# Kernel optimization log

Measured on AMD Instinct MI355X. Metric: run time of the kernel, lower is better.

The kernel has to match this reference:

```python
import jax, jax.numpy as jnp
import numpy as np

NUM_BINS = 31  # default num_bins in SummaryStats.from_array
N = 64 * 1024 * 1024  # 64M elements, 256 MB fp32 -> memory-bound reductions


def setup_inputs() -> dict:
    key = jax.random.key(0)
    x = jax.random.normal(key, (N,), dtype=jnp.float32)
    return {"x": x}


def reference(x):
    # SummaryStats.from_sharded_array on a single device (spec is fully replicated,
    # so _single_shard_histogram_array semantics apply: last bin is right-inclusive,
    # which matches jnp.histogram / searchsorted binning).
    x = x.ravel()
    mn = x.min()
    mx = x.max()
    nonzero_count = jnp.count_nonzero(x)
    num = jnp.asarray(x.size, dtype=nonzero_count.dtype)
    s = x.sum()
    ss = (x ** 2).sum()

    # histogram_bin_edges on stack([min, max]) with bins=NUM_BINS -> linspace(min, max, NUM_BINS+1)
    edges = jnp.linspace(mn, mx, NUM_BINS + 1)
    # bin index: values in [edges[i], edges[i+1]), last bin inclusive of edges[-1].
    idx = jnp.clip(jnp.searchsorted(edges, x, side="right") - 1, 0, NUM_BINS - 1)
    # exclude values strictly outside [min, max] (none here, but faithful to the compare logic)
    valid = (x >= edges[0]) & (x <= edges[-1])
    counts = jnp.zeros((NUM_BINS,), dtype=jnp.int32).at[idx].add(
        valid.astype(jnp.int32)
    )
    return mn, mx, num, nonzero_count, s, ss, counts, edges
```

## Files before the change

### kernel.cpp

```cpp
#include <hip/hip_runtime.h>

#define NBINS 31
#define NB1 2048
#define NB2 1024
#define PITCH 256

struct Partial {
    unsigned int mnk, mxk, nz, pad;
    double s, ss;
};
struct Finals {
    unsigned int minkey, maxkey;
    unsigned long long nz;
    double sum, ss;
};
#define OFF_F (NB1 * 32)
#define OFF_C (OFF_F + 64)

__device__ __forceinline__ unsigned int fkey(float f) {
    unsigned int u = __float_as_uint(f);
    return (u & 0x80000000u) ? ~u : (u | 0x80000000u);
}
__device__ __forceinline__ float funkey(unsigned int k) {
    return (k & 0x80000000u) ? __uint_as_float(k & 0x7FFFFFFFu)
                             : __uint_as_float(~k);
}
__device__ __forceinline__ float edge_at(float mn, float step, int i) {
    return __fadd_rn(mn, __fmul_rn((float)i, step));
}

__device__ __forceinline__ void acc4(float4 v, float& mn, float& mx, float& s, float& ss,
                                     unsigned int& nz) {
    mn = fminf(mn, fminf(fminf(v.x, v.y), fminf(v.z, v.w)));
    mx = fmaxf(mx, fmaxf(fmaxf(v.x, v.y), fmaxf(v.z, v.w)));
    s  += (v.x + v.y) + (v.z + v.w);
    ss += (v.x * v.x + v.y * v.y) + (v.z * v.z + v.w * v.w);
    nz += (v.x != 0.f) + (v.y != 0.f) + (v.z != 0.f) + (v.w != 0.f);
}

__global__ void __launch_bounds__(256) k_reduce(const float* __restrict__ x, long long n,
                                                Partial* __restrict__ part) {
    long long n4 = n >> 2;
    const float4* __restrict__ x4 = (const float4*)x;
    float mn = INFINITY, mx = -INFINITY, s = 0.f, ss = 0.f;
    unsigned int nz = 0u;

    long long stride = (long long)gridDim.x * blockDim.x;
    long long i = (long long)blockIdx.x * blockDim.x + threadIdx.x;
    for (; i + 3 * stride < n4; i += 4 * stride) {
        float4 a = x4[i], b = x4[i + stride], c = x4[i + 2 * stride], d = x4[i + 3 * stride];
        acc4(a, mn, mx, s, ss, nz);
        acc4(b, mn, mx, s, ss, nz);
        acc4(c, mn, mx, s, ss, nz);
        acc4(d, mn, mx, s, ss, nz);
    }
    for (; i < n4; i += stride) acc4(x4[i], mn, mx, s, ss, nz);
    if (blockIdx.x == 0 && threadIdx.x < (int)(n & 3)) {
        float v = x[(n4 << 2) + threadIdx.x];
        mn = fminf(mn, v); mx = fmaxf(mx, v);
        s += v; ss += v * v; nz += (v != 0.f);
    }

    double sd = (double)s, ssd = (double)ss;
    #pragma unroll
    for (int off = 32; off > 0; off >>= 1) {
        mn = fminf(mn, __shfl_down(mn, off));
        mx = fmaxf(mx, __shfl_down(mx, off));
        sd  += __shfl_down(sd, off);
        ssd += __shfl_down(ssd, off);
        nz  += __shfl_down(nz, off);
    }
    __shared__ float lmn[4], lmx[4];
    __shared__ double lsum[4], lss[4];
    __shared__ unsigned int lnz[4];
    int w = threadIdx.x >> 6;
    if ((threadIdx.x & 63) == 0) { lmn[w] = mn; lmx[w] = mx; lsum[w] = sd; lss[w] = ssd; lnz[w] = nz; }
    __syncthreads();
    if (threadIdx.x == 0) {
        Partial p;
        p.mnk = fkey(fminf(fminf(lmn[0], lmn[1]), fminf(lmn[2], lmn[3])));
        p.mxk = fkey(fmaxf(fmaxf(lmx[0], lmx[1]), fmaxf(lmx[2], lmx[3])));
        p.nz  = lnz[0] + lnz[1] + lnz[2] + lnz[3];
        p.pad = 0;
        p.s  = lsum[0] + lsum[1] + lsum[2] + lsum[3];
        p.ss = lss[0] + lss[1] + lss[2] + lss[3];
        part[blockIdx.x] = p;
    }
}

__global__ void __launch_bounds__(256) k_mid(const Partial* __restrict__ part,
                                             Finals* __restrict__ fin) {
    unsigned int mnk = 0xFFFFFFFFu, mxk = 0u;
    unsigned long long nz = 0ull;
    double s = 0.0, ss = 0.0;
    for (int i = threadIdx.x; i < NB1; i += 256) {
        Partial p = part[i];
        mnk = min(mnk, p.mnk); mxk = max(mxk, p.mxk);
        nz += p.nz; s += p.s; ss += p.ss;
    }
    #pragma unroll
    for (int off = 32; off > 0; off >>= 1) {
        mnk = min(mnk, __shfl_down(mnk, off));
        mxk = max(mxk, __shfl_down(mxk, off));
        nz += __shfl_down(nz, off);
        s  += __shfl_down(s, off);
        ss += __shfl_down(ss, off);
    }
    __shared__ unsigned int la[4], lb[4];
    __shared__ unsigned long long lnz[4];
    __shared__ double ls[4], lss[4];
    int w = threadIdx.x >> 6;
    if ((threadIdx.x & 63) == 0) { la[w] = mnk; lb[w] = mxk; lnz[w] = nz; ls[w] = s; lss[w] = ss; }
    __syncthreads();
    if (threadIdx.x == 0) {
        fin->minkey = min(min(la[0], la[1]), min(la[2], la[3]));
        fin->maxkey = max(max(lb[0], lb[1]), max(lb[2], lb[3]));
        fin->nz  = lnz[0] + lnz[1] + lnz[2] + lnz[3];
        fin->sum = ls[0] + ls[1] + ls[2] + ls[3];
        fin->ss  = lss[0] + lss[1] + lss[2] + lss[3];
    }
}

__device__ __forceinline__ void bump(float v, float mn, float inv,
                                     const float* __restrict__ E,
                                     unsigned int* __restrict__ hist, int tid) {
    int b = (int)((v - mn) * inv);
    b = b > 30 ? 30 : b;
    float lo = E[b];
    float hi = E[b + 1];
    b += (v >= hi);
    b -= (v < lo);
    b = b > 30 ? 30 : b;
    atomicAdd(&hist[(b << 8) + tid], 1u);
}

__global__ void __launch_bounds__(256) k_hist(const float* __restrict__ x, long long n,
                                              const Finals* __restrict__ fin,
                                              unsigned int* __restrict__ cpart) {
    __shared__ unsigned int hist[NBINS * PITCH];
    __shared__ float E[NBINS + 1];
    int tid = threadIdx.x;
    for (int j = tid; j < NBINS * PITCH; j += 256) hist[j] = 0u;

    float mn = funkey(fin->minkey);
    float mx = funkey(fin->maxkey);
    float step = (mx - mn) / 31.0f;
    float inv  = 31.0f / (mx - mn);
    if (tid < NBINS + 1) E[tid] = (tid == NBINS) ? mx : edge_at(mn, step, tid);
    __syncthreads();

    long long n4 = n >> 2;
    const float4* __restrict__ x4 = (const float4*)x;
    long long stride = (long long)gridDim.x * blockDim.x;
    long long i = (long long)blockIdx.x * blockDim.x + tid;
    for (; i + stride < n4; i += 2 * stride) {
        float4 a = x4[i], b = x4[i + stride];
        bump(a.x, mn, inv, E, hist, tid); bump(a.y, mn, inv, E, hist, tid);
        bump(a.z, mn, inv, E, hist, tid); bump(a.w, mn, inv, E, hist, tid);
        bump(b.x, mn, inv, E, hist, tid); bump(b.y, mn, inv, E, hist, tid);
        bump(b.z, mn, inv, E, hist, tid); bump(b.w, mn, inv, E, hist, tid);
    }
    for (; i < n4; i += stride) {
        float4 a = x4[i];
        bump(a.x, mn, inv, E, hist, tid); bump(a.y, mn, inv, E, hist, tid);
        bump(a.z, mn, inv, E, hist, tid); bump(a.w, mn, inv, E, hist, tid);
    }
    if (blockIdx.x == 0 && tid < (int)(n & 3))
        bump(x[(n4 << 2) + tid], mn, inv, E, hist, tid);
    __syncthreads();

    int w = tid >> 6, lane = tid & 63;
    for (int b = w; b < NBINS; b += 4) {
        const unsigned int* row = &hist[b * PITCH];
        uint4 q = *(const uint4*)(row + (lane << 2));
        unsigned int sv = q.x + q.y + q.z + q.w;
        #pragma unroll
        for (int off = 32; off > 0; off >>= 1) sv += __shfl_down(sv, off);
        if (lane == 0) cpart[b * NB2 + blockIdx.x] = sv;
    }
}

__global__ void __launch_bounds__(256) k_final(const Finals* __restrict__ fin,
                                               const unsigned int* __restrict__ cpart,
                                               float* __restrict__ out, long long n) {
    float mn = funkey(fin->minkey);
    float mx = funkey(fin->maxkey);
    float step = (mx - mn) / 31.0f;
    int w = threadIdx.x >> 6, lane = threadIdx.x & 63;
    for (int b = w; b < NBINS; b += 4) {
        const uint4* row = (const uint4*)(cpart + b * NB2);
        unsigned int sv = 0;
        for (int k = lane; k < NB2 / 4; k += 64) {
            uint4 q = row[k];
            sv += q.x + q.y + q.z + q.w;
        }
        #pragma unroll
        for (int off = 32; off > 0; off >>= 1) sv += __shfl_down(sv, off);
        if (lane == 0) out[6 + b] = (float)sv;
    }
    int t = threadIdx.x;
    if (t == 0) {
        out[0] = mn;
        out[1] = mx;
        out[2] = (float)n;
        out[3] = (float)fin->nz;
        out[4] = (float)fin->sum;
        out[5] = (float)fin->ss;
    }
    if (t < NBINS + 1) out[6 + NBINS + t] = (t == NBINS) ? mx : edge_at(mn, step, t);
}

extern "C" void kernel_launch(void* const* d_in, const int* in_sizes, int n_in,
                              void* d_out, int out_size, void* d_ws, size_t ws_size,
                              hipStream_t stream) {
    const float* x = (const float*)d_in[0];
    long long n = (long long)in_sizes[0];
    char* ws = (char*)d_ws;
    Partial* part = (Partial*)ws;
    Finals* fin = (Finals*)(ws + OFF_F);
    unsigned int* cpart = (unsigned int*)(ws + OFF_C);
    float* out = (float*)d_out;

    k_reduce<<<dim3(NB1), dim3(256), 0, stream>>>(x, n, part);
    k_mid<<<dim3(1), dim3(256), 0, stream>>>(part, fin);
    k_hist<<<dim3(NB2), dim3(256), 0, stream>>>(x, n, fin, cpart);
    k_final<<<dim3(1), dim3(256), 0, stream>>>(fin, cpart, out, n);
}
```

Before: 423.0 us.

## Fold mid and final reductions into histogram kernel, cutting launches to two

```diff
diff --git a/kernel.cpp b/kernel.cpp
--- a/kernel.cpp
+++ b/kernel.cpp
@@ -2,20 +2,15 @@
 
 #define NBINS 31
 #define NB1 2048
-#define NB2 1024
-#define PITCH 256
+#define NB2 2048
+#define HPITCH 128
 
 struct Partial {
     unsigned int mnk, mxk, nz, pad;
     double s, ss;
 };
-struct Finals {
-    unsigned int minkey, maxkey;
-    unsigned long long nz;
-    double sum, ss;
-};
-#define OFF_F (NB1 * 32)
-#define OFF_C (OFF_F + 64)
+#define OFF_G (NB1 * 32)
+#define OFF_CTR (OFF_G + 128)
 
 __device__ __forceinline__ unsigned int fkey(float f) {
     unsigned int u = __float_as_uint(f);
@@ -25,8 +20,8 @@
     return (k & 0x80000000u) ? __uint_as_float(k & 0x7FFFFFFFu)
                              : __uint_as_float(~k);
 }
-__device__ __forceinline__ float edge_at(float mn, float step, int i) {
-    return __fadd_rn(mn, __fmul_rn((float)i, step));
+__device__ __forceinline__ float edge_at(float mn, float step, float fi) {
+    return __fadd_rn(mn, __fmul_rn(fi, step));
 }
 
 __device__ __forceinline__ void acc4(float4 v, float& mn, float& mx, float& s, float& ss,
@@ -39,7 +34,14 @@
 }
 
 __global__ void __launch_bounds__(256) k_reduce(const float* __restrict__ x, long long n,
-                                                Partial* __restrict__ part) {
+                                                Partial* __restrict__ part,
+                                                unsigned int* __restrict__ ghist,
+                                                unsigned int* __restrict__ ctr) {
+    if (blockIdx.x == 0) {
+        if (threadIdx.x < NBINS) ghist[threadIdx.x] = 0u;
+        if (threadIdx.x == 32) *ctr = 0u;
+    }
+
     long long n4 = n >> 2;
     const float4* __restrict__ x4 = (const float4*)x;
     float mn = INFINITY, mx = -INFINITY, s = 0.f, ss = 0.f;
@@ -88,126 +90,115 @@
     }
 }
 
-__global__ void __launch_bounds__(256) k_mid(const Partial* __restrict__ part,
-                                             Finals* __restrict__ fin) {
+__device__ __forceinline__ void bump(float v, float mn, float step, float inv,
+                                     unsigned int* __restrict__ hist, int slot) {
+    int b = (int)((v - mn) * inv);
+    b = b > 30 ? 30 : b;
+    float bf = (float)b;
+    float lo = edge_at(mn, step, bf);
+    float hi = edge_at(mn, step, bf + 1.0f);
+    b += (v >= hi);
+    b -= (v < lo);
+    b = b > 30 ? 30 : b;
+    atomicAdd(&hist[(b << 7) + slot], 1u);
+}
+
+__global__ void __launch_bounds__(256) k_hist(const float* __restrict__ x, long long n,
+                                              const Partial* __restrict__ part,
+                                              unsigned int* __restrict__ ghist,
+                                              unsigned int* __restrict__ ctr,
+                                              float* __restrict__ out) {
+    __shared__ unsigned int hist[NBINS * HPITCH];
+    __shared__ unsigned int lmnk[4], lmxk[4];
+    __shared__ int islast;
+    int tid = threadIdx.x;
+    for (int j = tid; j < NBINS * HPITCH; j += 256) hist[j] = 0u;
+
     unsigned int mnk = 0xFFFFFFFFu, mxk = 0u;
-    unsigned long long nz = 0ull;
-    double s = 0.0, ss = 0.0;
-    for (int i = threadIdx.x; i < NB1; i += 256) {
-        Partial p = part[i];
-        mnk = min(mnk, p.mnk); mxk = max(mxk, p.mxk);
-        nz += p.nz; s += p.s; ss += p.ss;
+    for (int ii = tid; ii < NB1; ii += 256) {
+        uint2 p = *(const uint2*)&part[ii].mnk;
+        mnk = min(mnk, p.x); mxk = max(mxk, p.y);
     }
     #pragma unroll
     for (int off = 32; off > 0; off >>= 1) {
         mnk = min(mnk, __shfl_down(mnk, off));
         mxk = max(mxk, __shfl_down(mxk, off));
-        nz += __shfl_down(nz, off);
-        s  += __shfl_down(s, off);
-        ss += __shfl_down(ss, off);
-    }
-    __shared__ unsigned int la[4], lb[4];
-    __shared__ unsigned long long lnz[4];
-    __shared__ double ls[4], lss[4];
-    int w = threadIdx.x >> 6;
-    if ((threadIdx.x & 63) == 0) { la[w] = mnk; lb[w] = mxk; lnz[w] = nz; ls[w] = s; lss[w] = ss; }
-    __syncthreads();
-    if (threadIdx.x == 0) {
-        fin->minkey = min(min(la[0], la[1]), min(la[2], la[3]));
-        fin->maxkey = max(max(lb[0], lb[1]), max(lb[2], lb[3]));
-        fin->nz  = lnz[0] + lnz[1] + lnz[2] + lnz[3];
-        fin->sum = ls[0] + ls[1] + ls[2] + ls[3];
-        fin->ss  = lss[0] + lss[1] + lss[2] + lss[3];
-    }
-}
-
-__device__ __forceinline__ void bump(float v, float mn, float inv,
-                                     const float* __restrict__ E,
-                                     unsigned int* __restrict__ hist, int tid) {
-    int b = (int)((v - mn) * inv);
-    b = b > 30 ? 30 : b;
-    float lo = E[b];
-    float hi = E[b + 1];
-    b += (v >= hi);
-    b -= (v < lo);
-    b = b > 30 ? 30 : b;
-    atomicAdd(&hist[(b << 8) + tid], 1u);
-}
-
-__global__ void __launch_bounds__(256) k_hist(const float* __restrict__ x, long long n,
-                                              const Finals* __restrict__ fin,
-                                              unsigned int* __restrict__ cpart) {
-    __shared__ unsigned int hist[NBINS * PITCH];
-    __shared__ float E[NBINS + 1];
-    int tid = threadIdx.x;
-    for (int j = tid; j < NBINS * PITCH; j += 256) hist[j] = 0u;
-
-    float mn = funkey(fin->minkey);
-    float mx = funkey(fin->maxkey);
+    }
+    int w = tid >> 6;
+    if ((tid & 63) == 0) { lmnk[w] = mnk; lmxk[w] = mxk; }
+    __syncthreads();
+    float mn = funkey(min(min(lmnk[0], lmnk[1]), min(lmnk[2], lmnk[3])));
+    float mx = funkey(max(max(lmxk[0], lmxk[1]), max(lmxk[2], lmxk[3])));
     float step = (mx - mn) / 31.0f;
     float inv  = 31.0f / (mx - mn);
-    if (tid < NBINS + 1) E[tid] = (tid == NBINS) ? mx : edge_at(mn, step, tid);
-    __syncthreads();
-
+
+    if (blockIdx.x == 0) {
+        unsigned long long nz = 0ull; double s = 0.0, ss = 0.0;
+        for (int ii = tid; ii < NB1; ii += 256) {
+            Partial p = part[ii];
+            nz += p.nz; s += p.s; ss += p.ss;
+        }
+        #pragma unroll
+        for (int off = 32; off > 0; off >>= 1) {
+            nz += __shfl_down(nz, off);
+            s  += __shfl_down(s, off);
+            ss += __shfl_down(ss, off);
+        }
+        __shared__ unsigned long long lnz[4];
+        __shared__ double ls[4], lss2[4];
+        if ((tid & 63) == 0) { lnz[w] = nz; ls[w] = s; lss2[w] = ss; }
+        __syncthreads();
+        if (tid == 0) {
+            out[0] = mn;
+            out[1] = mx;
+            out[2] = (float)n;
+            out[3] = (float)(lnz[0] + lnz[1] + lnz[2] + lnz[3]);
+            out[4] = (float)(ls[0] + ls[1] + ls[2] + ls[3]);
+            out[5] = (float)(lss2[0] + lss2[1] + lss2[2] + lss2[3]);
+        }
+        if (tid < NBINS + 1)
+            out[6 + NBINS + tid] = (tid == NBINS) ? mx : edge_at(mn, step, (float)tid);
+    }
+
+    int slot = tid & (HPITCH - 1);
     long long n4 = n >> 2;
     const float4* __restrict__ x4 = (const float4*)x;
     long long stride = (long long)gridDim.x * blockDim.x;
     long long i = (long long)blockIdx.x * blockDim.x + tid;
     for (; i + stride < n4; i += 2 * stride) {
         float4 a = x4[i], b = x4[i + stride];
-        bump(a.x, mn, inv, E, hist, tid); bump(a.y, mn, inv, E, hist, tid);
-        bump(a.z, mn, inv, E, hist, tid); bump(a.w, mn, inv, E, hist, tid);
-        bump(b.x, mn, inv, E, hist, tid); bump(b.y, mn, inv, E, hist, tid);
-        bump(b.z, mn, inv, E, hist, tid); bump(b.w, mn, inv, E, hist, tid);
+        bump(a.x, mn, step, inv, hist, slot); bump(a.y, mn, step, inv, hist, slot);
+        bump(a.z, mn, step, inv, hist, slot); bump(a.w, mn, step, inv, hist, slot);
+        bump(b.x, mn, step, inv, hist, slot); bump(b.y, mn, step, inv, hist, slot);
+        bump(b.z, mn, step, inv, hist, slot); bump(b.w, mn, step, inv, hist, slot);
     }
     for (; i < n4; i += stride) {
         float4 a = x4[i];
-        bump(a.x, mn, inv, E, hist, tid); bump(a.y, mn, inv, E, hist, tid);
-        bump(a.z, mn, inv, E, hist, tid); bump(a.w, mn, inv, E, hist, tid);
+        bump(a.x, mn, step, inv, hist, slot); bump(a.y, mn, step, inv, hist, slot);
+        bump(a.z, mn, step, inv, hist, slot); bump(a.w, mn, step, inv, hist, slot);
     }
     if (blockIdx.x == 0 && tid < (int)(n & 3))
-        bump(x[(n4 << 2) + tid], mn, inv, E, hist, tid);
-    __syncthreads();
-
-    int w = tid >> 6, lane = tid & 63;
+        bump(x[(n4 << 2) + tid], mn, step, inv, hist, slot);
+    __syncthreads();
+
+    int lane = tid & 63;
     for (int b = w; b < NBINS; b += 4) {
-        const unsigned int* row = &hist[b * PITCH];
-        uint4 q = *(const uint4*)(row + (lane << 2));
-        unsigned int sv = q.x + q.y + q.z + q.w;
+        const unsigned int* row = &hist[b << 7];
+        uint2 q = *(const uint2*)(row + (lane << 1));
+        unsigned int sv = q.x + q.y;
         #pragma unroll
         for (int off = 32; off > 0; off >>= 1) sv += __shfl_down(sv, off);
-        if (lane == 0) cpart[b * NB2 + blockIdx.x] = sv;
-    }
-}
-
-__global__ void __launch_bounds__(256) k_final(const Finals* __restrict__ fin,
-                                               const unsigned int* __restrict__ cpart,
-                                               float* __restrict__ out, long long n) {
-    float mn = funkey(fin->minkey);
-    float mx = funkey(fin->maxkey);
-    float step = (mx - mn) / 31.0f;
-    int w = threadIdx.x >> 6, lane = threadIdx.x & 63;
-    for (int b = w; b < NBINS; b += 4) {
-        const uint4* row = (const uint4*)(cpart + b * NB2);
-        unsigned int sv = 0;
-        for (int k = lane; k < NB2 / 4; k += 64) {
-            uint4 q = row[k];
-            sv += q.x + q.y + q.z + q.w;
-        }
-        #pragma unroll
-        for (int off = 32; off > 0; off >>= 1) sv += __shfl_down(sv, off);
-        if (lane == 0) out[6 + b] = (float)sv;
-    }
-    int t = threadIdx.x;
-    if (t == 0) {
-        out[0] = mn;
-        out[1] = mx;
-        out[2] = (float)n;
-        out[3] = (float)fin->nz;
-        out[4] = (float)fin->sum;
-        out[5] = (float)fin->ss;
-    }
-    if (t < NBINS + 1) out[6 + NBINS + t] = (t == NBINS) ? mx : edge_at(mn, step, t);
+        if (lane == 0) atomicAdd(&ghist[b], sv);
+    }
+
+    __syncthreads();
+    if (tid == 0) {
+        __threadfence();
+        islast = (atomicAdd(ctr, 1u) == (unsigned int)(gridDim.x - 1));
+    }
+    __syncthreads();
+    if (islast && tid < NBINS)
+        out[6 + tid] = (float)atomicAdd(&ghist[tid], 0u);
 }
 
 extern "C" void kernel_launch(void* const* d_in, const int* in_sizes, int n_in,
@@ -217,12 +208,10 @@
     long long n = (long long)in_sizes[0];
     char* ws = (char*)d_ws;
     Partial* part = (Partial*)ws;
-    Finals* fin = (Finals*)(ws + OFF_F);
-    unsigned int* cpart = (unsigned int*)(ws + OFF_C);
+    unsigned int* ghist = (unsigned int*)(ws + OFF_G);
+    unsigned int* ctr = (unsigned int*)(ws + OFF_CTR);
     float* out = (float*)d_out;
 
-    k_reduce<<<dim3(NB1), dim3(256), 0, stream>>>(x, n, part);
-    k_mid<<<dim3(1), dim3(256), 0, stream>>>(part, fin);
-    k_hist<<<dim3(NB2), dim3(256), 0, stream>>>(x, n, fin, cpart);
-    k_final<<<dim3(1), dim3(256), 0, stream>>>(fin, cpart, out, n);
-}
+    k_reduce<<<dim3(NB1), dim3(256), 0, stream>>>(x, n, part, ghist, ctr);
+    k_hist<<<dim3(NB2), dim3(256), 0, stream>>>(x, n, part, ghist, ctr, out);
+}
```

Result: slower. 783.9 us (+85.3%).
